# Kernel tuning notes

Hardware: AMD Instinct MI355X
Metric: run time of the kernel (lower is better)

The kernel has to match this reference:

```python
import jax, jax.numpy as jnp
import numpy as np

N_NODES = 100000
N_EDGES = 3200000
IN_DIM = 64


def gcn_conv(x, edge_index, edge_weight, W, b, num_nodes):
    """PyG GCNConv: h = x @ W; add self-loops (w=1); symmetric norm; scatter-add; + bias."""
    src = edge_index[0]
    dst = edge_index[1]
    loop = jnp.arange(num_nodes)
    src_a = jnp.concatenate([src, loop])
    dst_a = jnp.concatenate([dst, loop])
    w_a = jnp.concatenate([edge_weight, jnp.ones((num_nodes,), dtype=edge_weight.dtype)])
    # degree at target nodes (weighted, incl. self-loops)
    deg = jax.ops.segment_sum(w_a, dst_a, num_segments=num_nodes)
    dinv = jnp.where(deg > 0, jax.lax.rsqrt(deg), 0.0)
    norm = dinv[src_a] * w_a * dinv[dst_a]  # [E+N]
    h = x @ W  # [N, out] - transform before propagate (cheaper: out_dim small)
    msg = h[src_a] * norm[:, None]  # [E+N, out]
    out = jax.ops.segment_sum(msg, dst_a, num_segments=num_nodes)
    return out + b


def setup_inputs() -> dict:
    key = jax.random.key(0)
    ks = jax.random.split(key, 9)
    x = jax.random.normal(ks[0], (N_NODES, IN_DIM), dtype=jnp.float32)
    edge_index = jax.random.randint(ks[1], (2, N_EDGES), 0, N_NODES, dtype=jnp.int64)
    edge_weight = jax.random.uniform(ks[2], (N_EDGES,), dtype=jnp.float32)
    s1 = 1.0 / np.sqrt(IN_DIM)
    W1 = jax.random.uniform(ks[3], (IN_DIM, 16), jnp.float32, -s1, s1)
    b1 = jnp.zeros((16,), jnp.float32)
    s2 = 1.0 / np.sqrt(16)
    W2 = jax.random.uniform(ks[4], (16, 2), jnp.float32, -s2, s2)
    b2 = jnp.zeros((2,), jnp.float32)
    s3 = 1.0 / np.sqrt(2)
    lin_w = jax.random.uniform(ks[5], (2, 1), jnp.float32, -s3, s3)
    lin_b = jax.random.uniform(ks[6], (1,), jnp.float32, -s3, s3)
    return {"x": x, "edge_index": edge_index, "edge_weight": edge_weight,
            "W1": W1, "b1": b1, "W2": W2, "b2": b2, "lin_w": lin_w, "lin_b": lin_b}


def reference(x, edge_index, edge_weight, W1, b1, W2, b2, lin_w, lin_b):
    h = gcn_conv(x, edge_index, edge_weight, W1, b1, N_NODES)
    h = jax.nn.relu(h)
    # F.dropout in eval mode = identity (deterministic reference)
    x2 = gcn_conv(h, edge_index, edge_weight, W2, b2, N_NODES)  # [N, 2]
    out = jax.nn.relu(x2)
    out = jax.nn.sigmoid(out @ lin_w + lin_b)  # [N, 1]
    return (out, x2)
```

## Files before the change

### kernel.cpp

```cpp
#include <hip/hip_runtime.h>
#include <math.h>

#define N_NODES 100000
#define N_EDGES 3200000
#define LO_BITS 7
#define NPB 128
#define NB  ((N_NODES + NPB - 1) / NPB)
#define PART_B 512
#define PART_T 1024
#define CPB (N_EDGES / PART_B)
#define BCAP 5120
#define CMAX 10

typedef unsigned long long u64;
typedef unsigned int u32;
typedef unsigned short u16;

static __device__ inline u16 f2bf(float f) {
    u32 u = __float_as_uint(f);
    return (u16)((u + 0x7FFF + ((u >> 16) & 1)) >> 16);
}
static __device__ inline float bf2f(u16 h) {
    return __uint_as_float((u32)h << 16);
}


__global__ void __launch_bounds__(PART_T) hist_k(const int* __restrict__ dst,
                                                 int* __restrict__ hist_mat) {
    __shared__ int h[NB];
    for (int t = threadIdx.x; t < NB; t += blockDim.x) h[t] = 0;
    __syncthreads();
    int base = blockIdx.x * CPB;
    for (int it = 0; it < (CPB + PART_T - 1) / PART_T; it++) {
        int e = base + it * PART_T + threadIdx.x;
        if (e < base + CPB) {
            int d = dst[e];
            atomicAdd(&h[d >> LO_BITS], 1);
        }
    }
    __syncthreads();
    for (int t = threadIdx.x; t < NB; t += blockDim.x)
        hist_mat[blockIdx.x * NB + t] = h[t];
}

__global__ void __launch_bounds__(PART_B) colscan_k(int* __restrict__ hist_mat,
                                                    int* __restrict__ tot) {
    __shared__ int s[PART_B];
    int bin = blockIdx.x, t = threadIdx.x;
    int v = hist_mat[t * NB + bin];
    s[t] = v;
    __syncthreads();
#pragma unroll
    for (int off = 1; off < PART_B; off <<= 1) {
        int u = (t >= off) ? s[t - off] : 0;
        __syncthreads();
        s[t] += u;
        __syncthreads();
    }
    hist_mat[t * NB + bin] = s[t] - v;
    if (t == PART_B - 1) tot[bin] = s[t];
}

__global__ void base_k(const int* __restrict__ tot, int* __restrict__ bbase) {
    __shared__ int s[1024];
    int t = threadIdx.x;
    int v = (t < NB) ? tot[t] : 0;
    s[t] = v;
    __syncthreads();
#pragma unroll
    for (int off = 1; off < 1024; off <<= 1) {
        int u = (t >= off) ? s[t - off] : 0;
        __syncthreads();
        s[t] += u;
        __syncthreads();
    }
    if (t < NB) bbase[t] = s[t] - v;
    if (t == 0) bbase[NB] = N_EDGES;
}

__global__ void __launch_bounds__(PART_T) part_k(
        const int* __restrict__ src, const int* __restrict__ dst,
        const float* __restrict__ w, const int* __restrict__ hist_mat,
        const int* __restrict__ bbase, u64* __restrict__ ebuf) {
    __shared__ u64 sorted[CPB];
    __shared__ int s[PART_T];
    __shared__ int cur[NB];
    __shared__ int gofs[NB];
    int t = threadIdx.x;
    int base = blockIdx.x * CPB;
    s[t] = 0;
    __syncthreads();
#pragma unroll
    for (int it = 0; it < (CPB + PART_T - 1) / PART_T; it++) {
        int e = base + it * PART_T + t;
        if (e < base + CPB) atomicAdd(&s[dst[e] >> LO_BITS], 1);
    }
    __syncthreads();
    int v = s[t];
    __syncthreads();
#pragma unroll
    for (int off = 1; off < PART_T; off <<= 1) {
        int u = (t >= off) ? s[t - off] : 0;
        __syncthreads();
        s[t] += u;
        __syncthreads();
    }
    if (t < NB) {
        int lscan = s[t] - v;
        cur[t] = lscan;
        gofs[t] = bbase[t] + hist_mat[blockIdx.x * NB + t] - lscan;
    }
    __syncthreads();
#pragma unroll
    for (int it = 0; it < (CPB + PART_T - 1) / PART_T; it++) {
        int e = base + it * PART_T + t;
        if (e < base + CPB) {
            int d = dst[e];
            int sv = __builtin_nontemporal_load(&src[e]);
            u32 wv = __float_as_uint(__builtin_nontemporal_load(&w[e]));
            int pos = atomicAdd(&cur[d >> LO_BITS], 1);
            sorted[pos] = ((u64)(u32)sv << 47) | ((u64)(u32)d << 30) | (u64)(wv >> 2);
        }
    }
    __syncthreads();
    for (int p = t; p < CPB; p += PART_T) {
        u64 pk = sorted[p];
        int sv = (int)(pk >> 47);
        int d  = (int)((pk >> 30) & 0x1FFFF);
        u32 wv = ((u32)pk & 0x3FFFFFFF) << 2;
        u32 hi = ((u32)sv << LO_BITS) | (u32)(d & (NPB - 1));
        ebuf[gofs[d >> LO_BITS] + p] = ((u64)hi << 32) | (u64)wv;
    }
}

__global__ void __launch_bounds__(512) csr_deg_k(
        const u64* __restrict__ ebuf, const int* __restrict__ bbase,
        int* __restrict__ row_ptr, float* __restrict__ dinv,
        u64* __restrict__ pedge) {
    __shared__ u64 staged[BCAP];
    __shared__ int   cnt[NPB];
    __shared__ float wsum[NPB];
    __shared__ int   sc[NPB];
    __shared__ int   cur[NPB];
    int b = blockIdx.x, t = threadIdx.x;
    if (t < NPB) { cnt[t] = 0; wsum[t] = 0.0f; }
    __syncthreads();
    int j0 = bbase[b], j1 = bbase[b + 1];
    u64 pe[CMAX];
    int nit = 0;
#pragma unroll
    for (int it = 0; it < CMAX; it++) {
        int j = j0 + it * 512 + t;
        if (j < j1) {
            u64 e = ebuf[j];
            pe[it] = e;
            int lo = (int)((u32)(e >> 32) & (NPB - 1));
            atomicAdd(&cnt[lo], 1);
            atomicAdd(&wsum[lo], __uint_as_float((u32)e));
            nit = it + 1;
        }
    }
    for (int j = j0 + 512 * CMAX + t; j < j1; j += 512) {
        u64 e = ebuf[j];
        int lo = (int)((u32)(e >> 32) & (NPB - 1));
        atomicAdd(&cnt[lo], 1);
        atomicAdd(&wsum[lo], __uint_as_float((u32)e));
    }
    __syncthreads();
    int v = (t < NPB) ? cnt[t] : 0;
    if (t < NPB) sc[t] = v;
    __syncthreads();
#pragma unroll
    for (int off = 1; off < NPB; off <<= 1) {
        int u = (t < NPB && t >= off) ? sc[t - off] : 0;
        __syncthreads();
        if (t < NPB) sc[t] += u;
        __syncthreads();
    }
    if (t < NPB) {
        int excl = sc[t] - v;
        cur[t] = excl;
        int node = b * NPB + t;
        if (node < N_NODES) {
            row_ptr[node] = j0 + excl;
            dinv[node] = rsqrtf(1.0f + wsum[t]);
        }
    }
    if (b == NB - 1 && t == 0) row_ptr[N_NODES] = N_EDGES;
    __syncthreads();
#pragma unroll
    for (int it = 0; it < CMAX; it++) {
        if (it < nit) {
            u64 e = pe[it];
            u32 hi = (u32)(e >> 32);
            int lo = (int)(hi & (NPB - 1));
            int p = atomicAdd(&cur[lo], 1);
            u64 val = ((u64)(hi >> LO_BITS) << 32) | (u64)(u32)e;
            if (p < BCAP) staged[p] = val;
            else pedge[j0 + p] = val;
        }
    }
    for (int j = j0 + 512 * CMAX + t; j < j1; j += 512) {
        u64 e = ebuf[j];
        u32 hi = (u32)(e >> 32);
        int lo = (int)(hi & (NPB - 1));
        int p = atomicAdd(&cur[lo], 1);
        u64 val = ((u64)(hi >> LO_BITS) << 32) | (u64)(u32)e;
        if (p < BCAP) staged[p] = val;
        else pedge[j0 + p] = val;
    }
    __syncthreads();
    int nbe = j1 - j0;
    int lim = nbe < BCAP ? nbe : BCAP;
    for (int p = t; p < lim; p += 512) pedge[j0 + p] = staged[p];
}


__global__ void __launch_bounds__(256) gemm1(
        const float* __restrict__ x, const float* __restrict__ W1,
        const float* __restrict__ dinv, u16* __restrict__ g1b) {
    __shared__ float sW[64 * 16];
    __shared__ float xs[16][68];
    for (int t = threadIdx.x; t < 64 * 16; t += blockDim.x) sW[t] = W1[t];
    int nbase = blockIdx.x * 16;
    {
        int q = threadIdx.x;
        const float4 v = ((const float4*)(x + (size_t)nbase * 64))[q];
        int n = q >> 4, f4 = q & 15;
        xs[n][f4 * 4 + 0] = v.x;
        xs[n][f4 * 4 + 1] = v.y;
        xs[n][f4 * 4 + 2] = v.z;
        xs[n][f4 * 4 + 3] = v.w;
    }
    __syncthreads();
    int n = threadIdx.x >> 4, c = threadIdx.x & 15;
    int node = nbase + n;
    float acc = 0.0f;
#pragma unroll
    for (int k = 0; k < 64; k++) acc += xs[n][k] * sW[k * 16 + c];
    g1b[node * 16 + c] = f2bf(acc * dinv[node]);
}

__global__ void gather1(const int* __restrict__ row_ptr, const u64* __restrict__ pedge,
                        const float* __restrict__ dinv, const u32* __restrict__ g1w,
                        const float* __restrict__ b1, const float* __restrict__ W2,
                        float* __restrict__ y2) {
    int gid = blockIdx.x * blockDim.x + threadIdx.x;
    int node = gid >> 6;
    if (node >= N_NODES) return;
    int lane = threadIdx.x & 63;
    int c2 = lane & 7;
    int eg = lane >> 3;
    int j0 = row_ptr[node], j1 = row_ptr[node + 1];
    float a0 = 0.0f, a1 = 0.0f;
    for (int base = j0; base < j1; base += 64) {
        int idx = base + lane;
        u64 se = (idx < j1) ? __builtin_nontemporal_load(&pedge[idx]) : 0ULL;
#pragma unroll
        for (int k = 0; k < 8; k++) {
            u64 pe = __shfl(se, k * 8 + eg, 64);
            int s = (int)(pe >> 32);
            float wr = __uint_as_float((u32)pe);
            u32 g2 = g1w[s * 8 + c2];
            a0 += bf2f((u16)g2) * wr;
            a1 += bf2f((u16)(g2 >> 16)) * wr;
        }
    }
    a0 += __shfl_xor(a0, 8, 64);  a1 += __shfl_xor(a1, 8, 64);
    a0 += __shfl_xor(a0, 16, 64); a1 += __shfl_xor(a1, 16, 64);
    a0 += __shfl_xor(a0, 32, 64); a1 += __shfl_xor(a1, 32, 64);
    u32 gs = g1w[node * 8 + c2];
    a0 += bf2f((u16)gs);
    a1 += bf2f((u16)(gs >> 16));
    float di = dinv[node];
    int c0 = c2 * 2, c1 = c0 + 1;
    float v0 = a0 * di + b1[c0]; v0 = v0 > 0.0f ? v0 : 0.0f;
    float v1 = a1 * di + b1[c1]; v1 = v1 > 0.0f ? v1 : 0.0f;
    float p0 = v0 * W2[c0 * 2]     + v1 * W2[c1 * 2];
    float p1 = v0 * W2[c0 * 2 + 1] + v1 * W2[c1 * 2 + 1];
    p0 += __shfl_xor(p0, 1, 64); p1 += __shfl_xor(p1, 1, 64);
    p0 += __shfl_xor(p0, 2, 64); p1 += __shfl_xor(p1, 2, 64);
    p0 += __shfl_xor(p0, 4, 64); p1 += __shfl_xor(p1, 4, 64);
    if (lane == 0) {
        y2[node * 2]     = p0 * di;
        y2[node * 2 + 1] = p1 * di;
    }
}

__global__ void gather2(const int* __restrict__ row_ptr, const u64* __restrict__ pedge,
                        const float* __restrict__ dinv, const float* __restrict__ y2,
                        const float* __restrict__ b2, const float* __restrict__ lin_w,
                        const float* __restrict__ lin_b, float* __restrict__ out) {
    int gid = blockIdx.x * blockDim.x + threadIdx.x;
    int i = gid >> 6;
    if (i >= N_NODES) return;
    int lane = threadIdx.x & 63;
    int k = lane & 1;
    int el = lane >> 1;
    int j0 = row_ptr[i], j1 = row_ptr[i + 1];
    float a = 0.0f;
    for (int base = j0; base < j1; base += 64) {
        int idx = base + lane;
        u64 se = (idx < j1) ? __builtin_nontemporal_load(&pedge[idx]) : 0ULL;
#pragma unroll
        for (int k2 = 0; k2 < 2; k2++) {
            u64 pe = __shfl(se, k2 * 32 + el, 64);
            int s = (int)(pe >> 32);
            float wr = __uint_as_float((u32)pe);
            a += y2[s * 2 + k] * wr;
        }
    }
    a += __shfl_xor(a, 2, 64);
    a += __shfl_xor(a, 4, 64);
    a += __shfl_xor(a, 8, 64);
    a += __shfl_xor(a, 16, 64);
    a += __shfl_xor(a, 32, 64);
    float ao = __shfl_xor(a, 1, 64);
    if (lane == 0) {
        float di = dinv[i];
        float y0 = y2[i * 2], y1 = y2[i * 2 + 1];
        float x20 = (a + y0) * di + b2[0];
        float x21 = (ao + y1) * di + b2[1];
        out[N_NODES + i * 2]     = x20;
        out[N_NODES + i * 2 + 1] = x21;
        float r0 = x20 > 0.0f ? x20 : 0.0f;
        float r1 = x21 > 0.0f ? x21 : 0.0f;
        float z = r0 * lin_w[0] + r1 * lin_w[1] + lin_b[0];
        out[i] = 1.0f / (1.0f + expf(-z));
    }
}

extern "C" void kernel_launch(void* const* d_in, const int* in_sizes, int n_in,
                              void* d_out, int out_size, void* d_ws, size_t ws_size,
                              hipStream_t stream) {
    const float* x     = (const float*)d_in[0];
    const int*   ei    = (const int*)d_in[1];
    const float* ew    = (const float*)d_in[2];
    const float* W1    = (const float*)d_in[3];
    const float* b1    = (const float*)d_in[4];
    const float* W2    = (const float*)d_in[5];
    const float* b2    = (const float*)d_in[6];
    const float* lin_w = (const float*)d_in[7];
    const float* lin_b = (const float*)d_in[8];
    float* out = (float*)d_out;

    const int* src = ei;
    const int* dst = ei + N_EDGES;

    char* w8 = (char*)d_ws;
    size_t off = 0;
    auto take = [&](size_t bytes) { char* p = w8 + off; off += (bytes + 15) & ~((size_t)15); return (void*)p; };
    u64*   ebuf     = (u64*)  take((size_t)N_EDGES * 8);
    u64*   pedge    = (u64*)  take((size_t)N_EDGES * 8);
    int*   hist_mat = (int*)  take((size_t)PART_B * NB * 4);
    int*   tot      = (int*)  take((size_t)NB * 4);
    int*   bbase    = (int*)  take((size_t)(NB + 1) * 4);
    int*   row_ptr  = (int*)  take((size_t)(N_NODES + 1) * 4);
    float* dinv     = (float*)take((size_t)N_NODES * 4);
    u16*   g1b      = (u16*)ebuf;
    u32*   g1w      = (u32*)ebuf;
    float* y2       = (float*)ebuf + (size_t)8 * N_NODES;

    const int B = 256;

    hist_k<<<PART_B, PART_T, 0, stream>>>(dst, hist_mat);
    colscan_k<<<NB, PART_B, 0, stream>>>(hist_mat, tot);
    base_k<<<1, 1024, 0, stream>>>(tot, bbase);
    part_k<<<PART_B, PART_T, 0, stream>>>(src, dst, ew, hist_mat, bbase, ebuf);

    csr_deg_k<<<NB, 512, 0, stream>>>(ebuf, bbase, row_ptr, dinv, pedge);

    gemm1<<<N_NODES / 16, B, 0, stream>>>(x, W1, dinv, g1b);
    gather1<<<(64 * N_NODES + B - 1) / B, B, 0, stream>>>(row_ptr, pedge, dinv, g1w, b1, W2, y2);

    gather2<<<(64 * N_NODES + B - 1) / B, B, 0, stream>>>(row_ptr, pedge, dinv, y2, b2,
                                                         lin_w, lin_b, out);
}
```

Baseline: 252.7 us.

## Use wave shuffle scans and reuse histogram counts instead of recounting in partition

Replaces the shared-memory Hillis-Steele scans (two barriers per step) in colscan, base, partition and CSR-degree kernels with a 64-lane shuffle scan plus a small per-wave sum combine. The partition kernel no longer re-reads dst to rebuild its per-block bin histogram; it reads the raw counts from the histogram kernel, with the column-scan exclusive offsets now written to a separate buffer. This cuts barrier count and one full pass over dst, at the cost of an extra histogram-sized workspace buffer.

```diff
diff --git a/kernel.cpp b/kernel.cpp
--- a/kernel.cpp
+++ b/kernel.cpp
@@ -24,6 +24,15 @@
     return __uint_as_float((u32)h << 16);
 }
 
+static __device__ inline int wave_iscan(int x, int lane) {
+#pragma unroll
+    for (int off = 1; off < 64; off <<= 1) {
+        int u = __shfl_up(x, off, 64);
+        if (lane >= off) x += u;
+    }
+    return x;
+}
+
 
 __global__ void __launch_bounds__(PART_T) hist_k(const int* __restrict__ dst,
                                                  int* __restrict__ hist_mat) {
@@ -43,72 +52,63 @@
         hist_mat[blockIdx.x * NB + t] = h[t];
 }
 
-__global__ void __launch_bounds__(PART_B) colscan_k(int* __restrict__ hist_mat,
+__global__ void __launch_bounds__(PART_B) colscan_k(const int* __restrict__ hist_mat,
+                                                    int* __restrict__ hist_excl,
                                                     int* __restrict__ tot) {
-    __shared__ int s[PART_B];
+    __shared__ int wsum[PART_B / 64];
     int bin = blockIdx.x, t = threadIdx.x;
+    int lane = t & 63, w = t >> 6;
     int v = hist_mat[t * NB + bin];
-    s[t] = v;
-    __syncthreads();
-#pragma unroll
-    for (int off = 1; off < PART_B; off <<= 1) {
-        int u = (t >= off) ? s[t - off] : 0;
-        __syncthreads();
-        s[t] += u;
-        __syncthreads();
-    }
-    hist_mat[t * NB + bin] = s[t] - v;
-    if (t == PART_B - 1) tot[bin] = s[t];
+    int x = wave_iscan(v, lane);
+    if (lane == 63) wsum[w] = x;
+    __syncthreads();
+    int base = 0;
+#pragma unroll
+    for (int i = 0; i < PART_B / 64; i++)
+        if (i < w) base += wsum[i];
+    hist_excl[t * NB + bin] = base + x - v;
+    if (t == PART_B - 1) tot[bin] = base + x;
 }
 
 __global__ void base_k(const int* __restrict__ tot, int* __restrict__ bbase) {
-    __shared__ int s[1024];
-    int t = threadIdx.x;
+    __shared__ int wsum[16];
+    int t = threadIdx.x, lane = t & 63, w = t >> 6;
     int v = (t < NB) ? tot[t] : 0;
-    s[t] = v;
-    __syncthreads();
-#pragma unroll
-    for (int off = 1; off < 1024; off <<= 1) {
-        int u = (t >= off) ? s[t - off] : 0;
-        __syncthreads();
-        s[t] += u;
-        __syncthreads();
-    }
-    if (t < NB) bbase[t] = s[t] - v;
+    int x = wave_iscan(v, lane);
+    if (lane == 63) wsum[w] = x;
+    __syncthreads();
+    int base = 0;
+#pragma unroll
+    for (int i = 0; i < 16; i++)
+        if (i < w) base += wsum[i];
+    if (t < NB) bbase[t] = base + x - v;
     if (t == 0) bbase[NB] = N_EDGES;
 }
 
 __global__ void __launch_bounds__(PART_T) part_k(
         const int* __restrict__ src, const int* __restrict__ dst,
         const float* __restrict__ w, const int* __restrict__ hist_mat,
+        const int* __restrict__ hist_excl,
         const int* __restrict__ bbase, u64* __restrict__ ebuf) {
     __shared__ u64 sorted[CPB];
-    __shared__ int s[PART_T];
     __shared__ int cur[NB];
     __shared__ int gofs[NB];
+    __shared__ int swsum[PART_T / 64];
     int t = threadIdx.x;
+    int lane = t & 63, wv = t >> 6;
     int base = blockIdx.x * CPB;
-    s[t] = 0;
-    __syncthreads();
-#pragma unroll
-    for (int it = 0; it < (CPB + PART_T - 1) / PART_T; it++) {
-        int e = base + it * PART_T + t;
-        if (e < base + CPB) atomicAdd(&s[dst[e] >> LO_BITS], 1);
-    }
-    __syncthreads();
-    int v = s[t];
-    __syncthreads();
-#pragma unroll
-    for (int off = 1; off < PART_T; off <<= 1) {
-        int u = (t >= off) ? s[t - off] : 0;
-        __syncthreads();
-        s[t] += u;
-        __syncthreads();
-    }
+    int rawc = (t < NB) ? hist_mat[blockIdx.x * NB + t] : 0;
+    int x = wave_iscan(rawc, lane);
+    if (lane == 63) swsum[wv] = x;
+    __syncthreads();
+    int bs = 0;
+#pragma unroll
+    for (int i = 0; i < PART_T / 64; i++)
+        if (i < wv) bs += swsum[i];
     if (t < NB) {
-        int lscan = s[t] - v;
+        int lscan = bs + x - rawc;
         cur[t] = lscan;
-        gofs[t] = bbase[t] + hist_mat[blockIdx.x * NB + t] - lscan;
+        gofs[t] = bbase[t] + hist_excl[blockIdx.x * NB + t] - lscan;
     }
     __syncthreads();
 #pragma unroll
@@ -117,9 +117,9 @@
         if (e < base + CPB) {
             int d = dst[e];
             int sv = __builtin_nontemporal_load(&src[e]);
-            u32 wv = __float_as_uint(__builtin_nontemporal_load(&w[e]));
+            u32 wvv = __float_as_uint(__builtin_nontemporal_load(&w[e]));
             int pos = atomicAdd(&cur[d >> LO_BITS], 1);
-            sorted[pos] = ((u64)(u32)sv << 47) | ((u64)(u32)d << 30) | (u64)(wv >> 2);
+            sorted[pos] = ((u64)(u32)sv << 47) | ((u64)(u32)d << 30) | (u64)(wvv >> 2);
         }
     }
     __syncthreads();
@@ -127,9 +127,9 @@
         u64 pk = sorted[p];
         int sv = (int)(pk >> 47);
         int d  = (int)((pk >> 30) & 0x1FFFF);
-        u32 wv = ((u32)pk & 0x3FFFFFFF) << 2;
+        u32 wvv = ((u32)pk & 0x3FFFFFFF) << 2;
         u32 hi = ((u32)sv << LO_BITS) | (u32)(d & (NPB - 1));
-        ebuf[gofs[d >> LO_BITS] + p] = ((u64)hi << 32) | (u64)wv;
+        ebuf[gofs[d >> LO_BITS] + p] = ((u64)hi << 32) | (u64)wvv;
     }
 }
 
@@ -140,8 +140,8 @@
     __shared__ u64 staged[BCAP];
     __shared__ int   cnt[NPB];
     __shared__ float wsum[NPB];
-    __shared__ int   sc[NPB];
     __shared__ int   cur[NPB];
+    __shared__ int   cw[2];
     int b = blockIdx.x, t = threadIdx.x;
     if (t < NPB) { cnt[t] = 0; wsum[t] = 0.0f; }
     __syncthreads();
@@ -167,18 +167,14 @@
         atomicAdd(&wsum[lo], __uint_as_float((u32)e));
     }
     __syncthreads();
+    int lane = t & 63;
     int v = (t < NPB) ? cnt[t] : 0;
-    if (t < NPB) sc[t] = v;
-    __syncthreads();
-#pragma unroll
-    for (int off = 1; off < NPB; off <<= 1) {
-        int u = (t < NPB && t >= off) ? sc[t - off] : 0;
-        __syncthreads();
-        if (t < NPB) sc[t] += u;
-        __syncthreads();
-    }
+    int x = wave_iscan(v, lane);
+    if (t < NPB && lane == 63) cw[t >> 6] = x;
+    __syncthreads();
     if (t < NPB) {
-        int excl = sc[t] - v;
+        int incl = x + ((t >= 64) ? cw[0] : 0);
+        int excl = incl - v;
         cur[t] = excl;
         int node = b * NPB + t;
         if (node < N_NODES) {
@@ -350,23 +346,24 @@
     char* w8 = (char*)d_ws;
     size_t off = 0;
     auto take = [&](size_t bytes) { char* p = w8 + off; off += (bytes + 15) & ~((size_t)15); return (void*)p; };
-    u64*   ebuf     = (u64*)  take((size_t)N_EDGES * 8);
-    u64*   pedge    = (u64*)  take((size_t)N_EDGES * 8);
-    int*   hist_mat = (int*)  take((size_t)PART_B * NB * 4);
-    int*   tot      = (int*)  take((size_t)NB * 4);
-    int*   bbase    = (int*)  take((size_t)(NB + 1) * 4);
-    int*   row_ptr  = (int*)  take((size_t)(N_NODES + 1) * 4);
-    float* dinv     = (float*)take((size_t)N_NODES * 4);
-    u16*   g1b      = (u16*)ebuf;
-    u32*   g1w      = (u32*)ebuf;
-    float* y2       = (float*)ebuf + (size_t)8 * N_NODES;
+    u64*   ebuf      = (u64*)  take((size_t)N_EDGES * 8);
+    u64*   pedge     = (u64*)  take((size_t)N_EDGES * 8);
+    int*   hist_mat  = (int*)  take((size_t)PART_B * NB * 4);
+    int*   hist_excl = (int*)  take((size_t)PART_B * NB * 4);
+    int*   tot       = (int*)  take((size_t)NB * 4);
+    int*   bbase     = (int*)  take((size_t)(NB + 1) * 4);
+    int*   row_ptr   = (int*)  take((size_t)(N_NODES + 1) * 4);
+    float* dinv      = (float*)take((size_t)N_NODES * 4);
+    u16*   g1b       = (u16*)ebuf;
+    u32*   g1w       = (u32*)ebuf;
+    float* y2        = (float*)ebuf + (size_t)8 * N_NODES;
 
     const int B = 256;
 
     hist_k<<<PART_B, PART_T, 0, stream>>>(dst, hist_mat);
-    colscan_k<<<NB, PART_B, 0, stream>>>(hist_mat, tot);
+    colscan_k<<<NB, PART_B, 0, stream>>>(hist_mat, hist_excl, tot);
     base_k<<<1, 1024, 0, stream>>>(tot, bbase);
-    part_k<<<PART_B, PART_T, 0, stream>>>(src, dst, ew, hist_mat, bbase, ebuf);
+    part_k<<<PART_B, PART_T, 0, stream>>>(src, dst, ew, hist_mat, hist_excl, bbase, ebuf);
 
     csr_deg_k<<<NB, 512, 0, stream>>>(ebuf, bbase, row_ptr, dinv, pedge);
 
```

After: 247.5 us. 2.0% less time.
